# Kernel tuning notes

Measured on AMD Instinct MI355X. Metric: run time of the kernel, lower is better.

Reference implementation:

```python
import jax, jax.numpy as jnp
import numpy as np

EMBED = 768
SPAT, TEMP, SYNC, GLOB, NEXP = 128, 64, 32, 64, 6


def _delta(x):
    # delta_i = x_i - x_{i-1}, with delta_0 = 0 (x_0 - x_0)
    x_shift = jnp.concatenate([x[:, :1, :], x[:, :-1, :]], axis=1)
    return x - x_shift


def setup_inputs() -> dict:
    key = jax.random.key(0)
    ks = jax.random.split(key, 13)
    B, S, D = 8, 4096, EMBED
    lim = lambda fan_in: 1.0 / np.sqrt(fan_in)
    u = lambda k, shp, fan_in: jax.random.uniform(k, shp, jnp.float32, -lim(fan_in), lim(fan_in))
    return {
        "x_text": jax.random.normal(ks[0], (B, S, D), jnp.float32),
        "x_au": jax.random.normal(ks[1], (B, S, D), jnp.float32),
        "x_vis": jax.random.normal(ks[2], (B, S, D), jnp.float32),
        "W_spat": u(ks[3], (3 * D, SPAT), 3 * D),
        "b_spat": u(ks[4], (SPAT,), 3 * D),
        "W_temp": u(ks[5], (3 * D, TEMP), 3 * D),
        "b_temp": u(ks[6], (TEMP,), 3 * D),
        "W_sync": u(ks[7], (D, SYNC), D),
        "b_sync": u(ks[8], (SYNC,), D),
        "W_glob": u(ks[9], (SPAT + TEMP + SYNC, GLOB), SPAT + TEMP + SYNC),
        "b_glob": u(ks[10], (GLOB,), SPAT + TEMP + SYNC),
        "W_route": u(ks[11], (SPAT + TEMP + SYNC + GLOB, NEXP), SPAT + TEMP + SYNC + GLOB),
        "b_route": u(ks[12], (NEXP,), SPAT + TEMP + SYNC + GLOB),
    }


def reference(x_text, x_au, x_vis, W_spat, b_spat, W_temp, b_temp,
              W_sync, b_sync, W_glob, b_glob, W_route, b_route):
    B, S, D = x_text.shape
    # local spatial: cat(text, au, vis) @ W_spat  -> (B,S,SPAT)
    spat_in = jnp.concatenate([x_text, x_au, x_vis], axis=-1)
    local_spat = jnp.einsum('bsf,fo->bso', spat_in, W_spat) + b_spat
    # local temporal: cat of first-order deltas -> (B,S,TEMP)
    temp_in = jnp.concatenate([_delta(x_text), _delta(x_au), _delta(x_vis)], axis=-1)
    local_temp = jnp.einsum('bsf,fo->bso', temp_in, W_temp) + b_temp
    # local sync: (au - vis) proj -> (B,S,SYNC)
    local_sync = jnp.einsum('bsf,fo->bso', x_au - x_vis, W_sync) + b_sync
    local_vec = jnp.concatenate([local_spat, local_temp, local_sync], axis=-1)
    # global context: mean over sequence of each local stream, then proj
    global_summary = jnp.mean(local_vec, axis=1)  # == cat of per-stream means
    global_vec = global_summary @ W_glob + b_glob  # (B,GLOB)
    # broadcast-concat + route projection
    glob_exp = jnp.broadcast_to(global_vec[:, None, :], (B, S, global_vec.shape[-1]))
    final_feat = jnp.concatenate([local_vec, glob_exp], axis=-1)
    gate_logits = jnp.einsum('bsf,fo->bso', final_feat, W_route) + b_route
    return gate_logits.reshape(-1, W_route.shape[-1])
```

## Files before the change

### kernel.cpp

```cpp
#include <hip/hip_runtime.h>
#include <hip/hip_bf16.h>

#define DIM 768
#define TD 2304
#define NB 8
#define NS 4096
#define NE 6

typedef __attribute__((ext_vector_type(8))) short bf16x8;
typedef __attribute__((ext_vector_type(4))) float f32x4;

#define OFF_BPK    0
#define OFF_A2F    36864
#define OFF_CB0    50688
#define OFF_ACCSUM 50704
#define OFF_CONSTB 50768
#define OFF_QP2    50832

__device__ __forceinline__ unsigned short f2bf(float f) {
    union { float f; unsigned u; } a; a.f = f;
    unsigned r = a.u + 0x7FFFu + ((a.u >> 16) & 1u);
    return (unsigned short)(r >> 16);
}

__device__ __forceinline__ bf16x8 pack8(float4 a, float4 b) {
    union { bf16x8 v; __hip_bfloat162 h[4]; } u;
    u.h[0] = __float22bfloat162_rn(make_float2(a.x, a.y));
    u.h[1] = __float22bfloat162_rn(make_float2(a.z, a.w));
    u.h[2] = __float22bfloat162_rn(make_float2(b.x, b.y));
    u.h[3] = __float22bfloat162_rn(make_float2(b.z, b.w));
    return u.v;
}

__global__ __launch_bounds__(256) void k_fold(
    const float* __restrict__ Wspat, const float* __restrict__ Wtemp,
    const float* __restrict__ Wsync, const float* __restrict__ Wroute,
    const float* __restrict__ Wglob, const float* __restrict__ bglob,
    const float* __restrict__ broute, const float* __restrict__ bspat,
    const float* __restrict__ btemp, const float* __restrict__ bsync,
    unsigned short* __restrict__ Bpk, float* __restrict__ A2F,
    float* __restrict__ cb0, float* __restrict__ accsum)
{
    __shared__ float lwr[288 * NE];
    __shared__ float lgf[224 * NE];
    const int t = threadIdx.x;
    for (int i = t; i < 288 * NE; i += 256) lwr[i] = Wroute[i];
    __syncthreads();
    if (t < 224) {
        float g[NE] = {0, 0, 0, 0, 0, 0};
        for (int o = 0; o < 64; ++o) {
            const float w = Wglob[t * 64 + o];
            #pragma unroll
            for (int e = 0; e < NE; ++e) g[e] += w * lwr[(224 + o) * NE + e];
        }
        #pragma unroll
        for (int e = 0; e < NE; ++e) lgf[t * NE + e] = g[e];
    }
    __syncthreads();
    if (blockIdx.x == 0) {
        if (t < NE) {
            float a = broute[t];
            for (int o = 0; o < 64; ++o)  a += bglob[o] * lwr[(224 + o) * NE + t];
            for (int o = 0; o < 128; ++o) a += bspat[o] * (lwr[o * NE + t] + lgf[o * NE + t]);
            for (int o = 0; o < 64; ++o)  a += btemp[o] * (lwr[(128 + o) * NE + t] + lgf[(128 + o) * NE + t]);
            for (int o = 0; o < 32; ++o)  a += bsync[o] * (lwr[(192 + o) * NE + t] + lgf[(192 + o) * NE + t]);
            cb0[t] = a;
        }
        if (t >= 128 && t < 192) accsum[t - 128] = 0.f;
    }

    const int d = blockIdx.x * 256 + t;
    const int st = d / DIM, dd = d - st * DIM;

    float p[NE] = {0, 0, 0, 0, 0, 0}, a2[NE] = {0, 0, 0, 0, 0, 0};
    for (int o = 0; o < 64; ++o) {
        const float w = Wtemp[d * 64 + o];
        #pragma unroll
        for (int e = 0; e < NE; ++e) {
            p[e]  += w * lwr[(128 + o) * NE + e];
            a2[e] += w * lgf[(128 + o) * NE + e];
        }
    }
    float qq[NE], a1[NE];
    #pragma unroll
    for (int e = 0; e < NE; ++e) { qq[e] = p[e]; a1[e] = 0.f; }
    for (int o = 0; o < 128; ++o) {
        const float w = Wspat[d * 128 + o];
        #pragma unroll
        for (int e = 0; e < NE; ++e) {
            qq[e] += w * lwr[o * NE + e];
            a1[e] += w * lgf[o * NE + e];
        }
    }
    if (st != 0) {
        const float sg = (st == 1) ? 1.f : -1.f;
        for (int o = 0; o < 32; ++o) {
            const float w = sg * Wsync[dd * 32 + o];
            #pragma unroll
            for (int e = 0; e < NE; ++e) {
                qq[e] += w * lwr[(192 + o) * NE + e];
                a1[e] += w * lgf[(192 + o) * NE + e];
            }
        }
    }
    const int ks = d >> 5, kk = d & 31;
    const int lh = (kk >> 3) * 16, j = kk & 7;
    unsigned short* b0 = Bpk + ks * 1024 + j;
    unsigned short* b1 = b0 + 512;
    #pragma unroll
    for (int e = 0; e < NE; ++e) {
        b0[(lh + e) * 8]     = f2bf(qq[e]);
        b0[(lh + 6 + e) * 8] = f2bf(p[e]);
        b1[(lh + e) * 8]     = f2bf(a1[e]);
        A2F[d * NE + e] = a2[e];
    }
}


#define GLDS(SRC, DST) \
    __builtin_amdgcn_global_load_lds((const __attribute__((address_space(1))) void*)(SRC), \
                                     (__attribute__((address_space(3))) void*)(DST), 16, 0, 0)

#define STAGE(DB, C) { \
    const int gc_ = khalf * 1152 + (C) * 64; \
    const int st_ = gc_ / DIM; \
    const float* Xp_ = (st_ == 0) ? xt : ((st_ == 1) ? xa : xv); \
    const float* base_ = Xp_ + (gc_ - st_ * DIM); \
    GLDS(base_ + soff0, &smem[(DB) * 4096 + (w * 16 + 0) * 64]); \
    GLDS(base_ + soff1, &smem[(DB) * 4096 + (w * 16 + 4) * 64]); \
    GLDS(base_ + soff2, &smem[(DB) * 4096 + (w * 16 + 8) * 64]); \
    GLDS(base_ + soff3, &smem[(DB) * 4096 + (w * 16 + 12) * 64]); }

#define BLOAD(C, B00, B01, B10, B11) { \
    const unsigned short* bp = Bpk + ((khalf * 18 + (C)) << 11) + (l << 3); \
    B00 = *(const bf16x8*)(bp); \
    B01 = *(const bf16x8*)(bp + 512); \
    B10 = *(const bf16x8*)(bp + 1024); \
    B11 = *(const bf16x8*)(bp + 1536); }

#define CMPT(DB, B00, B01, B10, B11) { \
    const float* ab_ = &smem[(DB) * 4096 + aoff]; \
    const float4 x0a = *(const float4*)(ab_ + u0f); \
    const float4 x0b = *(const float4*)(ab_ + u0f + 4); \
    const float4 x1a = *(const float4*)(ab_ + u1f); \
    const float4 x1b = *(const float4*)(ab_ + u1f + 4); \
    const bf16x8 fA0 = pack8(x0a, x0b); \
    const bf16x8 fA1 = pack8(x1a, x1b); \
    acc0 = __builtin_amdgcn_mfma_f32_16x16x32_bf16(fA0, B00, acc0, 0, 0, 0); \
    acc1 = __builtin_amdgcn_mfma_f32_16x16x32_bf16(fA0, B01, acc1, 0, 0, 0); \
    acc0 = __builtin_amdgcn_mfma_f32_16x16x32_bf16(fA1, B10, acc0, 0, 0, 0); \
    acc1 = __builtin_amdgcn_mfma_f32_16x16x32_bf16(fA1, B11, acc1, 0, 0, 0); }

__global__ __launch_bounds__(256, 4) void k_main(
    const float* __restrict__ xt, const float* __restrict__ xa, const float* __restrict__ xv,
    const unsigned short* __restrict__ Bpk, float* __restrict__ accsum,
    float* __restrict__ qp2)
{
    __shared__ float smem[2 * 64 * 64];
    const int t = threadIdx.x;
    const int l = t & 63;
    const int w = t >> 6;
    const int bid = blockIdx.x;
    const int khalf = bid & 1;
    const int rblk = bid >> 1;
    const int rb0 = rblk << 6;
    const int bb = rblk >> 6;

    const int u = l & 15;
    const int rsub = l >> 4;
    const int soff0 = (rb0 + w * 16 + 0  + rsub) * DIM + (u ^ ((( 0 + rsub) & 7) << 1)) * 4;
    const int soff1 = (rb0 + w * 16 + 4  + rsub) * DIM + (u ^ ((( 4 + rsub) & 7) << 1)) * 4;
    const int soff2 = (rb0 + w * 16 + 8  + rsub) * DIM + (u ^ ((( 8 + rsub) & 7) << 1)) * 4;
    const int soff3 = (rb0 + w * 16 + 12 + rsub) * DIM + (u ^ (((12 + rsub) & 7) << 1)) * 4;

    const int h2 = (l >> 4) * 2;
    const int swzr = ((l & 15) & 7) << 1;
    const int aoff = (w * 16 + (l & 15)) * 64;
    const int u0f = ((h2) ^ swzr) * 4;
    const int u1f = ((8 + h2) ^ swzr) * 4;

    f32x4 acc0 = {0.f, 0.f, 0.f, 0.f};
    f32x4 acc1 = {0.f, 0.f, 0.f, 0.f};
    bf16x8 B00, B01, B10, B11;

    STAGE(0, 0)

    #pragma unroll 1
    for (int c = 0; c < 17; ++c) {
        const int db = c & 1;
        BLOAD(c, B00, B01, B10, B11)
        __builtin_amdgcn_sched_barrier(0);
        STAGE(db ^ 1, c + 1)
        __builtin_amdgcn_sched_barrier(0);
        asm volatile("s_waitcnt vmcnt(4)" ::: "memory");
        __builtin_amdgcn_sched_barrier(0);
        CMPT(db, B00, B01, B10, B11)
    }
    BLOAD(17, B00, B01, B10, B11)
    asm volatile("s_waitcnt vmcnt(0)" ::: "memory");
    __builtin_amdgcn_sched_barrier(0);
    CMPT(1, B00, B01, B10, B11)

    const int c_out = l & 15, rgrp = l >> 4;
    float* qph = qp2 + (size_t)khalf * ((size_t)NB * NS * 12);
    if (c_out < 12) {
        const size_t rbase = (size_t)(rb0 + w * 16 + rgrp * 4) * 12 + c_out;
        qph[rbase]      = acc0[0];
        qph[rbase + 12] = acc0[1];
        qph[rbase + 24] = acc0[2];
        qph[rbase + 36] = acc0[3];
    }
    float v = acc1[0] + acc1[1] + acc1[2] + acc1[3];
    v += __shfl_xor(v, 16, 64);
    v += __shfl_xor(v, 32, 64);
    if (rgrp == 0 && c_out < 6)
        atomicAdd(&accsum[bb * NE + c_out], v);
}

__global__ __launch_bounds__(256) void k_const(
    const float* __restrict__ xt, const float* __restrict__ xa, const float* __restrict__ xv,
    const float* __restrict__ accsum, const float* __restrict__ A2F,
    const float* __restrict__ cb0, float* __restrict__ constb)
{
    const int b = blockIdx.x, t = threadIdx.x;
    float acc[NE] = {0, 0, 0, 0, 0, 0};
    for (int f = t; f < TD; f += 256) {
        const int st = f / DIM, dd = f - st * DIM;
        const float* Xp = ((st == 0) ? xt : ((st == 1) ? xa : xv)) + (size_t)b * NS * DIM;
        const float dm = Xp[(size_t)(NS - 1) * DIM + dd] - Xp[dd];
        const float* Ap = A2F + f * NE;
        #pragma unroll
        for (int e = 0; e < NE; ++e) acc[e] += dm * Ap[e];
    }
    #pragma unroll
    for (int e = 0; e < NE; ++e)
        for (int m = 1; m < 64; m <<= 1) acc[e] += __shfl_xor(acc[e], m, 64);
    __shared__ float wred[4][NE];
    if ((t & 63) == 0) {
        #pragma unroll
        for (int e = 0; e < NE; ++e) wred[t >> 6][e] = acc[e];
    }
    __syncthreads();
    if (t < NE) {
        const float inv = 1.f / 4096.f;
        const float dsum = wred[0][t] + wred[1][t] + wred[2][t] + wred[3][t];
        constb[b * NE + t] = cb0[t] + accsum[b * NE + t] * inv + dsum * inv;
    }
}

__global__ __launch_bounds__(256) void k_add(
    const float* __restrict__ qp2, const float* __restrict__ constb, float* __restrict__ out)
{
    const int row = blockIdx.x * 256 + threadIdx.x;
    const int b = row >> 12, s = row & (NS - 1);
    const int rowp = (s == 0) ? row : row - 1;
    const size_t H = (size_t)NB * NS * 12;
    const float* q0 = qp2 + (size_t)row * 12;
    const float* q1 = qp2 + H + (size_t)row * 12;
    const float* p0 = qp2 + (size_t)rowp * 12 + 6;
    const float* p1 = qp2 + H + (size_t)rowp * 12 + 6;
    float* op = out + (size_t)row * NE;
    #pragma unroll
    for (int e = 0; e < NE; ++e)
        op[e] = constb[b * NE + e] + q0[e] + q1[e] - p0[e] - p1[e];
}

extern "C" void kernel_launch(void* const* d_in, const int* in_sizes, int n_in,
                              void* d_out, int out_size, void* d_ws, size_t ws_size,
                              hipStream_t stream)
{
    const float* xt     = (const float*)d_in[0];
    const float* xa     = (const float*)d_in[1];
    const float* xv     = (const float*)d_in[2];
    const float* Wspat  = (const float*)d_in[3];
    const float* bspat  = (const float*)d_in[4];
    const float* Wtemp  = (const float*)d_in[5];
    const float* btemp  = (const float*)d_in[6];
    const float* Wsync  = (const float*)d_in[7];
    const float* bsync  = (const float*)d_in[8];
    const float* Wglob  = (const float*)d_in[9];
    const float* bglob  = (const float*)d_in[10];
    const float* Wroute = (const float*)d_in[11];
    const float* broute = (const float*)d_in[12];
    float* out = (float*)d_out;

    float* ws = (float*)d_ws;
    unsigned short* Bpk = (unsigned short*)(ws + OFF_BPK);
    float* A2F    = ws + OFF_A2F;
    float* cb0    = ws + OFF_CB0;
    float* accsum = ws + OFF_ACCSUM;
    float* constb = ws + OFF_CONSTB;
    float* qp2    = ws + OFF_QP2;

    hipMemsetAsync(Bpk, 0, 73728 * sizeof(unsigned short), stream);
    k_fold<<<9, 256, 0, stream>>>(Wspat, Wtemp, Wsync, Wroute, Wglob, bglob,
                                  broute, bspat, btemp, bsync, Bpk, A2F, cb0, accsum);
    k_main<<<1024, 256, 0, stream>>>(xt, xa, xv, Bpk, accsum, qp2);
    k_const<<<8, 256, 0, stream>>>(xt, xa, xv, accsum, A2F, cb0, constb);
    k_add<<<128, 256, 0, stream>>>(qp2, constb, out);
}
```

Before: 116.5 us.

## Deepen k_main pipeline to triple-buffered LDS with two-ahead prefetch

Replaces the double-buffered LDS staging loop with a triple-buffered ring that issues global-to-LDS loads two chunks ahead and prefetches B fragments one chunk ahead into alternating register sets. The loop is unrolled by six, and waitcnt thresholds are adjusted so more memory requests stay in flight during the MFMA work. The aim is to hide global load latency in this memory-bound GEMV-like kernel. It costs more LDS (48KB per block) and more registers, and lowers the launch-bounds occupancy hint from 4 to 3 blocks.

```diff
diff --git a/kernel.cpp b/kernel.cpp
--- a/kernel.cpp
+++ b/kernel.cpp
@@ -121,15 +121,15 @@
     __builtin_amdgcn_global_load_lds((const __attribute__((address_space(1))) void*)(SRC), \
                                      (__attribute__((address_space(3))) void*)(DST), 16, 0, 0)
 
-#define STAGE(DB, C) { \
+#define STAGE(BUF, C) { \
     const int gc_ = khalf * 1152 + (C) * 64; \
     const int st_ = gc_ / DIM; \
     const float* Xp_ = (st_ == 0) ? xt : ((st_ == 1) ? xa : xv); \
     const float* base_ = Xp_ + (gc_ - st_ * DIM); \
-    GLDS(base_ + soff0, &smem[(DB) * 4096 + (w * 16 + 0) * 64]); \
-    GLDS(base_ + soff1, &smem[(DB) * 4096 + (w * 16 + 4) * 64]); \
-    GLDS(base_ + soff2, &smem[(DB) * 4096 + (w * 16 + 8) * 64]); \
-    GLDS(base_ + soff3, &smem[(DB) * 4096 + (w * 16 + 12) * 64]); }
+    GLDS(base_ + soff0, &smem[(BUF) * 4096 + (w * 16 + 0) * 64]); \
+    GLDS(base_ + soff1, &smem[(BUF) * 4096 + (w * 16 + 4) * 64]); \
+    GLDS(base_ + soff2, &smem[(BUF) * 4096 + (w * 16 + 8) * 64]); \
+    GLDS(base_ + soff3, &smem[(BUF) * 4096 + (w * 16 + 12) * 64]); }
 
 #define BLOAD(C, B00, B01, B10, B11) { \
     const unsigned short* bp = Bpk + ((khalf * 18 + (C)) << 11) + (l << 3); \
@@ -138,8 +138,8 @@
     B10 = *(const bf16x8*)(bp + 1024); \
     B11 = *(const bf16x8*)(bp + 1536); }
 
-#define CMPT(DB, B00, B01, B10, B11) { \
-    const float* ab_ = &smem[(DB) * 4096 + aoff]; \
+#define CMPT(BUF, B00, B01, B10, B11) { \
+    const float* ab_ = &smem[(BUF) * 4096 + aoff]; \
     const float4 x0a = *(const float4*)(ab_ + u0f); \
     const float4 x0b = *(const float4*)(ab_ + u0f + 4); \
     const float4 x1a = *(const float4*)(ab_ + u1f); \
@@ -151,12 +151,21 @@
     acc0 = __builtin_amdgcn_mfma_f32_16x16x32_bf16(fA1, B10, acc0, 0, 0, 0); \
     acc1 = __builtin_amdgcn_mfma_f32_16x16x32_bf16(fA1, B11, acc1, 0, 0, 0); }
 
-__global__ __launch_bounds__(256, 4) void k_main(
+#define PHASE(C, BUFC, BUFS, CU00, CU01, CU10, CU11, NX00, NX01, NX10, NX11) \
+    BLOAD((C) + 1, NX00, NX01, NX10, NX11) \
+    __builtin_amdgcn_sched_barrier(0); \
+    STAGE(BUFS, (C) + 2) \
+    __builtin_amdgcn_sched_barrier(0); \
+    asm volatile("s_waitcnt vmcnt(12)" ::: "memory"); \
+    __builtin_amdgcn_sched_barrier(0); \
+    CMPT(BUFC, CU00, CU01, CU10, CU11)
+
+__global__ __launch_bounds__(256, 3) void k_main(
     const float* __restrict__ xt, const float* __restrict__ xa, const float* __restrict__ xv,
     const unsigned short* __restrict__ Bpk, float* __restrict__ accsum,
     float* __restrict__ qp2)
 {
-    __shared__ float smem[2 * 64 * 64];
+    __shared__ float smem[3 * 64 * 64];
     const int t = threadIdx.x;
     const int l = t & 63;
     const int w = t >> 6;
@@ -181,25 +190,36 @@
 
     f32x4 acc0 = {0.f, 0.f, 0.f, 0.f};
     f32x4 acc1 = {0.f, 0.f, 0.f, 0.f};
-    bf16x8 B00, B01, B10, B11;
+    bf16x8 A00, A01, A10, A11, Bb00, Bb01, Bb10, Bb11;
 
     STAGE(0, 0)
+    __builtin_amdgcn_sched_barrier(0);
+    BLOAD(0, A00, A01, A10, A11)
+    __builtin_amdgcn_sched_barrier(0);
+    STAGE(1, 1)
+    __builtin_amdgcn_sched_barrier(0);
 
     #pragma unroll 1
-    for (int c = 0; c < 17; ++c) {
-        const int db = c & 1;
-        BLOAD(c, B00, B01, B10, B11)
-        __builtin_amdgcn_sched_barrier(0);
-        STAGE(db ^ 1, c + 1)
-        __builtin_amdgcn_sched_barrier(0);
-        asm volatile("s_waitcnt vmcnt(4)" ::: "memory");
-        __builtin_amdgcn_sched_barrier(0);
-        CMPT(db, B00, B01, B10, B11)
-    }
-    BLOAD(17, B00, B01, B10, B11)
+    for (int base = 0; base < 12; base += 6) {
+        PHASE(base + 0, 0, 2, A00, A01, A10, A11, Bb00, Bb01, Bb10, Bb11)
+        PHASE(base + 1, 1, 0, Bb00, Bb01, Bb10, Bb11, A00, A01, A10, A11)
+        PHASE(base + 2, 2, 1, A00, A01, A10, A11, Bb00, Bb01, Bb10, Bb11)
+        PHASE(base + 3, 0, 2, Bb00, Bb01, Bb10, Bb11, A00, A01, A10, A11)
+        PHASE(base + 4, 1, 0, A00, A01, A10, A11, Bb00, Bb01, Bb10, Bb11)
+        PHASE(base + 5, 2, 1, Bb00, Bb01, Bb10, Bb11, A00, A01, A10, A11)
+    }
+    PHASE(12, 0, 2, A00, A01, A10, A11, Bb00, Bb01, Bb10, Bb11)
+    PHASE(13, 1, 0, Bb00, Bb01, Bb10, Bb11, A00, A01, A10, A11)
+    PHASE(14, 2, 1, A00, A01, A10, A11, Bb00, Bb01, Bb10, Bb11)
+    PHASE(15, 0, 2, Bb00, Bb01, Bb10, Bb11, A00, A01, A10, A11)
+    BLOAD(17, Bb00, Bb01, Bb10, Bb11)
+    __builtin_amdgcn_sched_barrier(0);
+    asm volatile("s_waitcnt vmcnt(8)" ::: "memory");
+    __builtin_amdgcn_sched_barrier(0);
+    CMPT(1, A00, A01, A10, A11)
     asm volatile("s_waitcnt vmcnt(0)" ::: "memory");
     __builtin_amdgcn_sched_barrier(0);
-    CMPT(1, B00, B01, B10, B11)
+    CMPT(2, Bb00, Bb01, Bb10, Bb11)
 
     const int c_out = l & 15, rgrp = l >> 4;
     float* qph = qp2 + (size_t)khalf * ((size_t)NB * NS * 12);
```

New measurement: 120.9 us. +3.7%, slower.
